# Kernel optimization log

Hardware: AMD Instinct MI355X
Metric: run time of the kernel (lower is better)

The kernel has to match this reference:

```python
import jax, jax.numpy as jnp
import numpy as np
import math

THETA = 10000.0

def apply_rope(x):
    # x: [B, H, S, D] with D even; interleaved even/odd rotation
    B, H, S, D = x.shape
    dim_half = D // 2
    freq_idx = jnp.arange(dim_half, dtype=jnp.float32)
    inv_freq = jnp.exp(-math.log(THETA) * freq_idx * 2.0 / D)  # [D/2]
    pos = jnp.arange(S, dtype=jnp.float32)
    angles = pos[:, None] * inv_freq[None, :]      # [S, D/2]
    cos = jnp.cos(angles)[None, None]              # [1,1,S,D/2]
    sin = jnp.sin(angles)[None, None]
    x_even = x[..., ::2]
    x_odd = x[..., 1::2]
    r_even = x_even * cos - x_odd * sin
    r_odd = x_odd * cos + x_even * sin
    return jnp.stack([r_even, r_odd], axis=-1).reshape(B, H, S, D)

def setup_inputs() -> dict:
    key = jax.random.key(0)
    ks = jax.random.split(key, 5)
    B, S, E = 2, 2048, 1024
    std = 0.02
    inp = {
        "hidden_states": jax.random.normal(ks[0], (B, S, E), dtype=jnp.float32),
        "Wq": jax.random.normal(ks[1], (E, E), dtype=jnp.float32) * std,
        "bq": jnp.zeros((E,), dtype=jnp.float32),
        "Wk": jax.random.normal(ks[2], (E, E), dtype=jnp.float32) * std,
        "bk": jnp.zeros((E,), dtype=jnp.float32),
        "Wv": jax.random.normal(ks[3], (E, E), dtype=jnp.float32) * std,
        "bv": jnp.zeros((E,), dtype=jnp.float32),
        "Wo": jax.random.normal(ks[4], (E, E), dtype=jnp.float32) * std,
        "bo": jnp.zeros((E,), dtype=jnp.float32),
    }
    return inp

def reference(hidden_states, Wq, bq, Wk, bk, Wv, bv, Wo, bo):
    NUM_HEADS = 16
    B, S, E = hidden_states.shape
    D = E // NUM_HEADS
    scale = 1.0 / math.sqrt(D)

    def proj(W, b):
        # torch Linear: x @ W.T + b; then [B,S,H,D] -> [B,H,S,D]
        y = hidden_states @ W.T + b
        return y.reshape(B, S, NUM_HEADS, D).transpose(0, 2, 1, 3)

    q = apply_rope(proj(Wq, bq))
    k = apply_rope(proj(Wk, bk))
    v = proj(Wv, bv)

    scores = jnp.einsum("bhqd,bhkd->bhqk", q, k) * scale
    attn = jax.nn.softmax(scores, axis=-1)
    out = jnp.einsum("bhqk,bhkd->bhqd", attn, v)  # [B,H,S,D]
    out = out.transpose(0, 2, 1, 3).reshape(B, S, E)
    return out @ Wo.T + bo  # dropout: eval mode (identity)
```

## Files before the change

kernel.cpp:

```cpp
#include <hip/hip_runtime.h>
#include <hip/hip_bf16.h>
#include <math.h>

#define B_ 2
#define S_ 2048
#define E_ 1024
#define H_ 16
#define D_ 64
#define M_ (B_*S_)
#define PT 32

typedef short bf16x8 __attribute__((ext_vector_type(8)));
typedef float f32x4 __attribute__((ext_vector_type(4)));
typedef unsigned short u16x4 __attribute__((ext_vector_type(4)));

#define SCLQ 0.18033688011112042f

__device__ __forceinline__ unsigned short f2bf(float f) {
    unsigned int u = __builtin_bit_cast(unsigned int, f);
    u += 0x7FFFu + ((u >> 16) & 1u);
    return (unsigned short)(u >> 16);
}
__device__ __forceinline__ unsigned int pk2bf(float a, float b) {
    __hip_bfloat162 h = __float22bfloat162_rn(make_float2(a, b));
    unsigned int u;
    __builtin_memcpy(&u, &h, 4);
    return u;
}
__device__ __forceinline__ f32x4 mfma16(bf16x8 a, bf16x8 b, f32x4 c) {
    return __builtin_amdgcn_mfma_f32_16x16x32_bf16(a, b, c, 0, 0, 0);
}
__device__ __forceinline__ bf16x8 cvt8(const float* p) {
    f32x4 lo = *(const f32x4*)p;
    f32x4 hi = *(const f32x4*)(p + 4);
    unsigned int pk[4];
    pk[0] = pk2bf(lo[0], lo[1]);
    pk[1] = pk2bf(lo[2], lo[3]);
    pk[2] = pk2bf(hi[0], hi[1]);
    pk[3] = pk2bf(hi[2], hi[3]);
    bf16x8 r;
    __builtin_memcpy(&r, pk, 16);
    return r;
}
__device__ __forceinline__ void g2l16(const unsigned short* g, unsigned short* l) {
    __builtin_amdgcn_global_load_lds(
        (const __attribute__((address_space(1))) unsigned int*)(const void*)g,
        (__attribute__((address_space(3))) unsigned int*)(void*)l,
        16, 0, 0);
}

__global__ __launch_bounds__(256) void cvt_kernel(
    const float* __restrict__ X,  const float* __restrict__ Wq,
    const float* __restrict__ Wk, const float* __restrict__ Wv,
    const float* __restrict__ Wo,
    unsigned short* __restrict__ Xb, unsigned short* __restrict__ Wb,
    float* __restrict__ tab)
{
    const int y = blockIdx.y;
    if (y == 5) {
        unsigned int i = blockIdx.x * 256 + threadIdx.x;
        if (i < 32 * 2048) {
            int f = i >> 11, s = i & 2047;
            const float C = -0.41524101186091903f;
            const float INV2PI = 0.15915494309189535f;
            float inv_rev = exp2f(C * (float)f) * INV2PI;
            float rev = (float)s * inv_rev;
            float fr = rev - rintf(rev);
            tab[i]           = __builtin_amdgcn_cosf(fr);
            tab[65536 + i]   = __builtin_amdgcn_sinf(fr);
        }
        return;
    }
    const float* src = (y == 0) ? X : (y == 1) ? Wq : (y == 2) ? Wk : (y == 3) ? Wv : Wo;
    unsigned short* dst = (y == 0) ? Xb : Wb + (size_t)(y - 1) * (E_ * E_);
    const size_t n = (y == 0) ? (size_t)M_ * E_ : (size_t)E_ * E_;
    size_t i = ((size_t)blockIdx.x * 256 + threadIdx.x) * 8;
    if (i < n) *(bf16x8*)(dst + i) = cvt8(src + i);
}

__global__ __launch_bounds__(256, 4) void qkv_rope_bf(
    const unsigned short* __restrict__ Xb, const unsigned short* __restrict__ Wb,
    const float* __restrict__ bq, const float* __restrict__ bk,
    const float* __restrict__ bv, const float* __restrict__ tab,
    unsigned short* __restrict__ Qo, unsigned short* __restrict__ Ko,
    unsigned short* __restrict__ Vo)
{
    __shared__ __align__(16) unsigned char lds_raw[128 * 132 * 2];
    unsigned short* As = (unsigned short*)lds_raw;
    unsigned short* Bs = (unsigned short*)(lds_raw + 8192);
    unsigned short* Cs = (unsigned short*)lds_raw;

    const int t = threadIdx.x;
    const int w = t >> 6, lane = t & 63, quad = lane >> 4, l16 = lane & 15;
    const int wr = (w >> 1) * 64, wc = (w & 1) * 64;
    const int n0 = blockIdx.x * 128, m0 = blockIdx.y * 128;
    const int z = blockIdx.z;
    const unsigned short* W = Wb + (size_t)z * (E_ * E_);
    const float* bias = (z == 0) ? bq : (z == 1) ? bk : bv;

    const int r4 = t >> 2, c8 = (t & 3) * 8;
    const unsigned short* Ag = Xb + (size_t)(m0 + r4) * E_ + c8;
    const unsigned short* Bg = W  + (size_t)(n0 + r4) * E_ + c8;

    f32x4 zero = {0.f, 0.f, 0.f, 0.f};
    f32x4 acc[4][4];
#pragma unroll
    for (int i = 0; i < 4; i++)
#pragma unroll
        for (int j = 0; j < 4; j++) acc[i][j] = zero;

    for (int kt = 0; kt < E_; kt += 32) {
        __syncthreads();
        g2l16(Ag + kt,           &As[t * 8]);
        g2l16(Ag + 64 * E_ + kt, &As[t * 8 + 2048]);
        g2l16(Bg + kt,           &Bs[t * 8]);
        g2l16(Bg + 64 * E_ + kt, &Bs[t * 8 + 2048]);
        __syncthreads();
        bf16x8 af[4], bfr[4];
#pragma unroll
        for (int i = 0; i < 4; i++)
            af[i] = *(const bf16x8*)&As[(wr + i * 16 + l16) * 32 + quad * 8];
#pragma unroll
        for (int j = 0; j < 4; j++)
            bfr[j] = *(const bf16x8*)&Bs[(wc + j * 16 + l16) * 32 + quad * 8];
#pragma unroll
        for (int i = 0; i < 4; i++)
#pragma unroll
            for (int j = 0; j < 4; j++)
                acc[i][j] = mfma16(af[i], bfr[j], acc[i][j]);
    }

    __syncthreads();
    const int seg = quad;
    if (z < 2) {
        const float qscale = (z == 0) ? SCLQ : 1.0f;
#pragma unroll
        for (int j = 0; j < 4; j++) {
            int n_local = wc + j * 16 + l16;
            int n = n0 + n_local;
            int d = n & 63, f = d >> 1;
            float bvv = bias[n];
            float sgn = (d & 1) ? 1.f : -1.f;
            const float* ct = tab + f * 2048;
            const float* st_ = tab + 65536 + f * 2048;
#pragma unroll
            for (int i = 0; i < 4; i++) {
                int mb = wr + i * 16 + quad * 4;
                int sb = (m0 + mb) & (S_ - 1);
                f32x4 cs4 = *(const f32x4*)&ct[sb];
                f32x4 sn4 = *(const f32x4*)&st_[sb];
#pragma unroll
                for (int r = 0; r < 4; r++) {
                    float val = acc[i][j][r] + bvv;
                    float oth = __shfl_xor(val, 1);
                    Cs[(mb + r) * 132 + n_local] =
                        f2bf((val * cs4[r] + sgn * oth * sn4[r]) * qscale);
                }
            }
        }
        __syncthreads();
        unsigned short* Out = (z == 0) ? Qo : Ko;
        const int btok = m0 >> 11;
        const int half = seg & 1;
#pragma unroll
        for (int it = 0; it < 16; it++) {
            int m_local = it * 8 + w * 2 + (seg >> 1);
            int s = (m0 + m_local) & (S_ - 1);
            int h = (n0 + half * 64) >> 6;
            u16x4 v = *(const u16x4*)&Cs[m_local * 132 + half * 64 + l16 * 4];
            *(u16x4*)&Out[(((size_t)btok * H_ + h) * S_ + s) * D_ + l16 * 4] = v;
        }
    } else {
#pragma unroll
        for (int j = 0; j < 4; j++) {
            int n_local = wc + j * 16 + l16;
            float bvv = bias[n0 + n_local];
#pragma unroll
            for (int i = 0; i < 4; i++) {
                int mb = wr + i * 16 + quad * 4;
#pragma unroll
                for (int r = 0; r < 4; r++)
                    Cs[n_local * 132 + mb + r] = f2bf(acc[i][j][r] + bvv);
            }
        }
        __syncthreads();
        const int btok = m0 >> 11;
        const int s0 = m0 & (S_ - 1);
        const int half = seg & 1;
#pragma unroll
        for (int it = 0; it < 16; it++) {
            int n_local = it * 8 + w * 2 + (seg >> 1);
            int n = n0 + n_local;
            int h = n >> 6, d = n & 63;
            u16x4 v = *(const u16x4*)&Cs[n_local * 132 + half * 64 + l16 * 4];
            *(u16x4*)&Vo[(((size_t)btok * H_ + h) * D_ + d) * S_ + s0 + half * 64 + l16 * 4] = v;
        }
    }
}

__global__ __launch_bounds__(512, 2) void attn_direct(
    const unsigned short* __restrict__ Q, const unsigned short* __restrict__ K,
    const unsigned short* __restrict__ Vt, unsigned short* __restrict__ ctx)
{
    __shared__ unsigned short Ks[3][64 * 64];
    __shared__ unsigned short Vs[3][64 * 64];
    __shared__ unsigned short Ps[8][16 * 72];
    const int t = threadIdx.x;
    const int w = t >> 6, lane = t & 63, quad = lane >> 4, l16 = lane & 15;
    const int bh = blockIdx.y;
    const int q0 = blockIdx.x * 128 + w * 16;
    const int NT = S_ / 64;

    const unsigned short* Qg = Q + ((size_t)bh * S_ + q0) * D_;
    bf16x8 qf[2];
#pragma unroll
    for (int ks = 0; ks < 2; ks++)
        qf[ks] = *(const bf16x8*)(Qg + (size_t)l16 * 64 + ks * 32 + quad * 8);

    bf16x8 ones;
#pragma unroll
    for (int e = 0; e < 8; e++) ones[e] = (short)0x3F80;

    f32x4 zero = {0.f, 0.f, 0.f, 0.f};
    f32x4 acc_o[4];
    f32x4 acc_l = zero;
#pragma unroll
    for (int j = 0; j < 4; j++) acc_o[j] = zero;

    const int tt = t & 255, ksel = t >> 8;
    const int sr = tt >> 2;
    const int sc = ((tt & 3) ^ ((tt >> 3) & 3)) * 8;
    const unsigned short* KgL = K  + (size_t)bh * S_ * D_ + (size_t)sr * 64 + ksel * 32 + sc;
    const unsigned short* VgL = Vt + (size_t)bh * D_ * S_ + (size_t)sr * S_ + ksel * 32 + sc;

    const int sl = (quad ^ ((l16 >> 1) & 3)) * 8;

    g2l16(KgL, &Ks[0][t * 8]);
    g2l16(VgL, &Vs[0][t * 8]);
    __syncthreads();
    g2l16(KgL + 4096, &Ks[1][t * 8]);
    g2l16(VgL + 64,   &Vs[1][t * 8]);
    {
        f32x4 sc4[4];
#pragma unroll
        for (int j = 0; j < 4; j++) sc4[j] = zero;
#pragma unroll
        for (int ks = 0; ks < 2; ks++)
#pragma unroll
            for (int j = 0; j < 4; j++) {
                bf16x8 kf = *(const bf16x8*)&Ks[0][ks * 2048 + (j * 16 + l16) * 32 + sl];
                sc4[j] = mfma16(qf[ks], kf, sc4[j]);
            }
#pragma unroll
        for (int j = 0; j < 4; j++)
#pragma unroll
            for (int r = 0; r < 4; r += 2) {
                float pa = __builtin_amdgcn_exp2f(sc4[j][r]);
                float pb = __builtin_amdgcn_exp2f(sc4[j][r + 1]);
                unsigned int u = pk2bf(pa, pb);
                Ps[w][(quad * 4 + r)     * 72 + j * 16 + l16] = (unsigned short)u;
                Ps[w][(quad * 4 + r + 1) * 72 + j * 16 + l16] = (unsigned short)(u >> 16);
            }
    }

    int bc = 0, bn = 1, bx = 2;
    for (int i = 0; i < NT - 1; ++i) {
        __syncthreads();
        if (i + 2 < NT) {
            g2l16(KgL + (size_t)(i + 2) * 4096, &Ks[bx][t * 8]);
            g2l16(VgL + (i + 2) * 64,           &Vs[bx][t * 8]);
        }
        bf16x8 pf0 = *(const bf16x8*)&Ps[w][l16 * 72 + quad * 8];
        bf16x8 pf1 = *(const bf16x8*)&Ps[w][l16 * 72 + 32 + quad * 8];

        __builtin_amdgcn_s_setprio(1);
        f32x4 scn[4];
#pragma unroll
        for (int j = 0; j < 4; j++) scn[j] = zero;
#pragma unroll
        for (int ks = 0; ks < 2; ks++)
#pragma unroll
            for (int j = 0; j < 4; j++) {
                bf16x8 kf = *(const bf16x8*)&Ks[bn][ks * 2048 + (j * 16 + l16) * 32 + sl];
                scn[j] = mfma16(qf[ks], kf, scn[j]);
            }
#pragma unroll
        for (int jd = 0; jd < 4; jd++) {
            bf16x8 vf = *(const bf16x8*)&Vs[bc][(jd * 16 + l16) * 32 + sl];
            acc_o[jd] = mfma16(pf0, vf, acc_o[jd]);
        }
        acc_l = mfma16(pf0, ones, acc_l);
#pragma unroll
        for (int jd = 0; jd < 4; jd++) {
            bf16x8 vf = *(const bf16x8*)&Vs[bc][2048 + (jd * 16 + l16) * 32 + sl];
            acc_o[jd] = mfma16(pf1, vf, acc_o[jd]);
        }
        acc_l = mfma16(pf1, ones, acc_l);
        __builtin_amdgcn_s_setprio(0);

#pragma unroll
        for (int j = 0; j < 4; j++)
#pragma unroll
            for (int r = 0; r < 4; r += 2) {
                float pa = __builtin_amdgcn_exp2f(scn[j][r]);
                float pb = __builtin_amdgcn_exp2f(scn[j][r + 1]);
                unsigned int u = pk2bf(pa, pb);
                Ps[w][(quad * 4 + r)     * 72 + j * 16 + l16] = (unsigned short)u;
                Ps[w][(quad * 4 + r + 1) * 72 + j * 16 + l16] = (unsigned short)(u >> 16);
            }

        int tb = bc; bc = bn; bn = bx; bx = tb;
    }

    {
        bf16x8 pf0 = *(const bf16x8*)&Ps[w][l16 * 72 + quad * 8];
        bf16x8 pf1 = *(const bf16x8*)&Ps[w][l16 * 72 + 32 + quad * 8];
#pragma unroll
        for (int jd = 0; jd < 4; jd++) {
            bf16x8 vf = *(const bf16x8*)&Vs[bc][(jd * 16 + l16) * 32 + sl];
            acc_o[jd] = mfma16(pf0, vf, acc_o[jd]);
        }
        acc_l = mfma16(pf0, ones, acc_l);
#pragma unroll
        for (int jd = 0; jd < 4; jd++) {
            bf16x8 vf = *(const bf16x8*)&Vs[bc][2048 + (jd * 16 + l16) * 32 + sl];
            acc_o[jd] = mfma16(pf1, vf, acc_o[jd]);
        }
        acc_l = mfma16(pf1, ones, acc_l);
    }

    const int b = bh >> 4, h = bh & 15;
    f32x4 rl;
#pragma unroll
    for (int r = 0; r < 4; r++) rl[r] = 1.0f / acc_l[r];
#pragma unroll
    for (int jd = 0; jd < 4; jd++)
#pragma unroll
        for (int r = 0; r < 4; r++) {
            int qrow = q0 + quad * 4 + r;
            int col = h * 64 + jd * 16 + l16;
            ctx[((size_t)b * S_ + qrow) * E_ + col] = f2bf(acc_o[jd][r] * rl[r]);
        }
}

__global__ __launch_bounds__(256, 4) void out_bf(
    const unsigned short* __restrict__ Cx, const unsigned short* __restrict__ Wob,
    const float* __restrict__ bo, float* __restrict__ out)
{
    __shared__ unsigned short As[128 * 32];
    __shared__ unsigned short Bs[64 * 32];
    const int t = threadIdx.x;
    const int w = t >> 6, lane = t & 63, quad = lane >> 4, l16 = lane & 15;
    const int m0 = blockIdx.y * 128, n0 = blockIdx.x * 64;
    const int wr = w * 32;
    const int r4 = t >> 2, c8 = (t & 3) * 8;
    const unsigned short* Ag = Cx  + (size_t)(m0 + r4) * E_ + c8;
    const unsigned short* Bg = Wob + (size_t)(n0 + r4) * E_ + c8;

    f32x4 zero = {0.f, 0.f, 0.f, 0.f};
    f32x4 acc[2][4];
#pragma unroll
    for (int i = 0; i < 2; i++)
#pragma unroll
        for (int j = 0; j < 4; j++) acc[i][j] = zero;

    for (int kt = 0; kt < E_; kt += 32) {
        __syncthreads();
        g2l16(Ag + kt,           &As[t * 8]);
        g2l16(Ag + 64 * E_ + kt, &As[t * 8 + 2048]);
        g2l16(Bg + kt,           &Bs[t * 8]);
        __syncthreads();
        bf16x8 af[2], bfr[4];
#pragma unroll
        for (int i = 0; i < 2; i++)
            af[i] = *(const bf16x8*)&As[(wr + i * 16 + l16) * 32 + quad * 8];
#pragma unroll
        for (int j = 0; j < 4; j++)
            bfr[j] = *(const bf16x8*)&Bs[(j * 16 + l16) * 32 + quad * 8];
#pragma unroll
        for (int i = 0; i < 2; i++)
#pragma unroll
            for (int j = 0; j < 4; j++)
                acc[i][j] = mfma16(af[i], bfr[j], acc[i][j]);
    }

#pragma unroll
    for (int j = 0; j < 4; j++) {
        int n = n0 + j * 16 + l16;
        float bvv = bo[n];
#pragma unroll
        for (int i = 0; i < 2; i++) {
            int mrow = m0 + wr + i * 16 + quad * 4;
#pragma unroll
            for (int r = 0; r < 4; r++)
                out[(size_t)(mrow + r) * E_ + n] = acc[i][j][r] + bvv;
        }
    }
}

__global__ __launch_bounds__(256, 3) void qkv_rope_f32(
    const float* __restrict__ X,
    const float* __restrict__ Wq, const float* __restrict__ Wk,
    const float* __restrict__ Wv,
    const float* __restrict__ bq, const float* __restrict__ bk,
    const float* __restrict__ bv,
    unsigned short* __restrict__ Qo, unsigned short* __restrict__ Ko,
    unsigned short* __restrict__ Vo)
{
    __shared__ __align__(16) unsigned char lds_raw[128 * 132 * 2];
    unsigned short* As = (unsigned short*)lds_raw;
    unsigned short* Bs = (unsigned short*)(lds_raw + 8192);
    unsigned short* Cs = (unsigned short*)lds_raw;

    const int t = threadIdx.x;
    const int w = t >> 6, lane = t & 63, quad = lane >> 4, l16 = lane & 15;
    const int wr = (w >> 1) * 64, wc = (w & 1) * 64;
    const int n0 = blockIdx.x * 128, m0 = blockIdx.y * 128;
    const int z = blockIdx.z;
    const float* W    = (z == 0) ? Wq : (z == 1) ? Wk : Wv;
    const float* bias = (z == 0) ? bq : (z == 1) ? bk : bv;

    const int r4 = t >> 2, c8 = (t & 3) * 8;
    const int st = r4 * PT + c8;
    const float* Ag = X + (size_t)(m0 + r4) * E_ + c8;
    const float* Bg = W + (size_t)(n0 + r4) * E_ + c8;

    f32x4 zero = {0.f, 0.f, 0.f, 0.f};
    f32x4 acc[4][4];
#pragma unroll
    for (int i = 0; i < 4; i++)
#pragma unroll
        for (int j = 0; j < 4; j++) acc[i][j] = zero;

    for (int kt = 0; kt < E_; kt += 32) {
        bf16x8 a0 = cvt8(Ag + kt);
        bf16x8 a1 = cvt8(Ag + 64 * E_ + kt);
        bf16x8 b0 = cvt8(Bg + kt);
        bf16x8 b1 = cvt8(Bg + 64 * E_ + kt);
        __syncthreads();
        *(bf16x8*)&As[st]           = a0;
        *(bf16x8*)&As[st + 64 * PT] = a1;
        *(bf16x8*)&Bs[st]           = b0;
        *(bf16x8*)&Bs[st + 64 * PT] = b1;
        __syncthreads();
        bf16x8 af[4], bfr[4];
#pragma unroll
        for (int i = 0; i < 4; i++)
            af[i] = *(const bf16x8*)&As[(wr + i * 16 + l16) * PT + quad * 8];
#pragma unroll
        for (int j = 0; j < 4; j++)
            bfr[j] = *(const bf16x8*)&Bs[(wc + j * 16 + l16) * PT + quad * 8];
#pragma unroll
        for (int i = 0; i < 4; i++)
#pragma unroll
            for (int j = 0; j < 4; j++)
                acc[i][j] = mfma16(af[i], bfr[j], acc[i][j]);
    }

    __syncthreads();
    const int seg = quad;
    if (z < 2) {
        const float C = -0.41524101186091903f;
        const float INV2PI = 0.15915494309189535f;
        const float qscale = (z == 0) ? SCLQ : 1.0f;
#pragma unroll
        for (int j = 0; j < 4; j++) {
            int n_local = wc + j * 16 + l16;
            int n = n0 + n_local;
            int d = n & 63, f = d >> 1;
            float inv_rev = exp2f(C * (float)f) * INV2PI;
            float bvv = bias[n];
            float sgn = (d & 1) ? 1.f : -1.f;
#pragma unroll
            for (int i = 0; i < 4; i++) {
                int mb = wr + i * 16 + quad * 4;
#pragma unroll
                for (int r = 0; r < 4; r++) {
                    int m = m0 + mb + r;
                    int s = m & (S_ - 1);
                    float val = acc[i][j][r] + bvv;
                    float oth = __shfl_xor(val, 1);
                    float rev = (float)s * inv_rev;
                    float fr = rev - rintf(rev);
                    float sn = __builtin_amdgcn_sinf(fr);
                    float cs = __builtin_amdgcn_cosf(fr);
                    Cs[(mb + r) * 132 + n_local] =
                        f2bf((val * cs + sgn * oth * sn) * qscale);
                }
            }
        }
        __syncthreads();
        unsigned short* Out = (z == 0) ? Qo : Ko;
        const int btok = m0 >> 11;
        const int half = seg & 1;
#pragma unroll
        for (int it = 0; it < 16; it++) {
            int m_local = it * 8 + w * 2 + (seg >> 1);
            int s = (m0 + m_local) & (S_ - 1);
            int h = (n0 + half * 64) >> 6;
            u16x4 v = *(const u16x4*)&Cs[m_local * 132 + half * 64 + l16 * 4];
            *(u16x4*)&Out[(((size_t)btok * H_ + h) * S_ + s) * D_ + l16 * 4] = v;
        }
    } else {
#pragma unroll
        for (int j = 0; j < 4; j++) {
            int n_local = wc + j * 16 + l16;
            float bvv = bias[n0 + n_local];
#pragma unroll
            for (int i = 0; i < 4; i++) {
                int mb = wr + i * 16 + quad * 4;
#pragma unroll
                for (int r = 0; r < 4; r++)
                    Cs[n_local * 132 + mb + r] = f2bf(acc[i][j][r] + bvv);
            }
        }
        __syncthreads();
        const int btok = m0 >> 11;
        const int s0 = m0 & (S_ - 1);
        const int half = seg & 1;
#pragma unroll
        for (int it = 0; it < 16; it++) {
            int n_local = it * 8 + w * 2 + (seg >> 1);
            int n = n0 + n_local;
            int h = n >> 6, d = n & 63;
            u16x4 v = *(const u16x4*)&Cs[n_local * 132 + half * 64 + l16 * 4];
            *(u16x4*)&Vo[(((size_t)btok * H_ + h) * D_ + d) * S_ + s0 + half * 64 + l16 * 4] = v;
        }
    }
}

__global__ __launch_bounds__(256, 2) void out_f32(
    const unsigned short* __restrict__ Cx, const float* __restrict__ Wo,
    const float* __restrict__ bo, float* __restrict__ out)
{
    __shared__ unsigned short As[128 * PT];
    __shared__ unsigned short Bs[64 * PT];
    const int t = threadIdx.x;
    const int w = t >> 6, lane = t & 63, quad = lane >> 4, l16 = lane & 15;
    const int m0 = blockIdx.y * 128, n0 = blockIdx.x * 64;
    const int wr = w * 32;
    const int r4 = t >> 2, c8 = (t & 3) * 8;
    const int st = r4 * PT + c8;
    const unsigned short* Ag = Cx + (size_t)(m0 + r4) * E_ + c8;
    const float*          Bg = Wo + (size_t)(n0 + (r4 & 63)) * E_ + c8;

    f32x4 zero = {0.f, 0.f, 0.f, 0.f};
    f32x4 acc[2][4];
#pragma unroll
    for (int i = 0; i < 2; i++)
#pragma unroll
        for (int j = 0; j < 4; j++) acc[i][j] = zero;

    for (int kt = 0; kt < E_; kt += 32) {
        bf16x8 a0 = *(const bf16x8*)(Ag + kt);
        bf16x8 a1 = *(const bf16x8*)(Ag + 64 * E_ + kt);
        bf16x8 b0 = cvt8(Bg + kt);
        __syncthreads();
        *(bf16x8*)&As[st]           = a0;
        *(bf16x8*)&As[st + 64 * PT] = a1;
        *(bf16x8*)&Bs[st]           = b0;
        __syncthreads();
        bf16x8 af[2], bfr[4];
#pragma unroll
        for (int i = 0; i < 2; i++)
            af[i] = *(const bf16x8*)&As[(wr + i * 16 + l16) * PT + quad * 8];
#pragma unroll
        for (int j = 0; j < 4; j++)
            bfr[j] = *(const bf16x8*)&Bs[(j * 16 + l16) * PT + quad * 8];
#pragma unroll
        for (int i = 0; i < 2; i++)
#pragma unroll
            for (int j = 0; j < 4; j++)
                acc[i][j] = mfma16(af[i], bfr[j], acc[i][j]);
    }

#pragma unroll
    for (int j = 0; j < 4; j++) {
        int n = n0 + j * 16 + l16;
        float bvv = bo[n];
#pragma unroll
        for (int i = 0; i < 2; i++) {
            int mrow = m0 + wr + i * 16 + quad * 4;
#pragma unroll
            for (int r = 0; r < 4; r++)
                out[(size_t)(mrow + r) * E_ + n] = acc[i][j][r] + bvv;
        }
    }
}

extern "C" void kernel_launch(void* const* d_in, const int* in_sizes, int n_in,
                              void* d_out, int out_size, void* d_ws, size_t ws_size,
                              hipStream_t stream) {
    const float* X  = (const float*)d_in[0];
    const float* Wq = (const float*)d_in[1];
    const float* bq = (const float*)d_in[2];
    const float* Wk = (const float*)d_in[3];
    const float* bk = (const float*)d_in[4];
    const float* Wv = (const float*)d_in[5];
    const float* bv = (const float*)d_in[6];
    const float* Wo = (const float*)d_in[7];
    const float* bo = (const float*)d_in[8];
    float* outp = (float*)d_out;

    const size_t TN = (size_t)B_ * H_ * S_ * D_;
    const size_t need_f32 = 4 * TN * sizeof(unsigned short);
    const size_t need_bf  = 5 * TN * sizeof(unsigned short) + 2 * 65536 * sizeof(float);
    if (ws_size < need_f32) return;

    unsigned short* Qb = (unsigned short*)d_ws;
    unsigned short* Kb = Qb + TN;
    unsigned short* Vb = Kb + TN;

    if (ws_size >= need_bf) {
        unsigned short* Xb = Vb + TN;
        unsigned short* Wb = Xb + TN;
        float* tab = (float*)(Wb + 4 * (size_t)(E_ * E_));
        unsigned short* Cx = Xb;

        cvt_kernel<<<dim3(2048, 6), 256, 0, stream>>>(X, Wq, Wk, Wv, Wo, Xb, Wb, tab);
        qkv_rope_bf<<<dim3(E_ / 128, M_ / 128, 3), 256, 0, stream>>>(
            Xb, Wb, bq, bk, bv, tab, Qb, Kb, Vb);
        attn_direct<<<dim3(S_ / 128, B_ * H_), 512, 0, stream>>>(Qb, Kb, Vb, Cx);
        out_bf<<<dim3(E_ / 64, M_ / 128), 256, 0, stream>>>(
            Cx, Wb + 3 * (size_t)(E_ * E_), bo, outp);
    } else {
        unsigned short* Cx = Vb + TN;
        qkv_rope_f32<<<dim3(E_ / 128, M_ / 128, 3), 256, 0, stream>>>(
            X, Wq, Wk, Wv, bq, bk, bv, Qb, Kb, Vb);
        attn_direct<<<dim3(S_ / 128, B_ * H_), 512, 0, stream>>>(Qb, Kb, Vb, Cx);
        out_f32<<<dim3(E_ / 64, M_ / 128), 256, 0, stream>>>(Cx, Wo, bo, outp);
    }
}
```

Measured before the change: 191.7 us.

## Process two 16-row query groups per wave in attention to reuse K/V fragments

Each wave in the attention kernel now handles 32 query rows (two 16-row groups) instead of 16, and each block covers 256 queries. Every K and V fragment read from LDS feeds two MFMAs, halving LDS fragment traffic per FLOP and halving global K/V tile loads per query. The grid shrinks to 256 blocks, which lowers parallelism on a GPU with many CUs, and register pressure rises from the doubled accumulators.

```diff
diff --git a/kernel.cpp b/kernel.cpp
--- a/kernel.cpp
+++ b/kernel.cpp
@@ -204,28 +204,32 @@
 {
     __shared__ unsigned short Ks[3][64 * 64];
     __shared__ unsigned short Vs[3][64 * 64];
-    __shared__ unsigned short Ps[8][16 * 72];
+    __shared__ unsigned short Ps[8][32 * 72];
     const int t = threadIdx.x;
     const int w = t >> 6, lane = t & 63, quad = lane >> 4, l16 = lane & 15;
     const int bh = blockIdx.y;
-    const int q0 = blockIdx.x * 128 + w * 16;
+    const int q0 = blockIdx.x * 256 + w * 32;
     const int NT = S_ / 64;
 
     const unsigned short* Qg = Q + ((size_t)bh * S_ + q0) * D_;
-    bf16x8 qf[2];
-#pragma unroll
-    for (int ks = 0; ks < 2; ks++)
-        qf[ks] = *(const bf16x8*)(Qg + (size_t)l16 * 64 + ks * 32 + quad * 8);
+    bf16x8 qf[2][2];
+#pragma unroll
+    for (int rg = 0; rg < 2; rg++)
+#pragma unroll
+        for (int ks = 0; ks < 2; ks++)
+            qf[rg][ks] = *(const bf16x8*)(Qg + (size_t)(rg * 16 + l16) * 64 + ks * 32 + quad * 8);
 
     bf16x8 ones;
 #pragma unroll
     for (int e = 0; e < 8; e++) ones[e] = (short)0x3F80;
 
     f32x4 zero = {0.f, 0.f, 0.f, 0.f};
-    f32x4 acc_o[4];
-    f32x4 acc_l = zero;
-#pragma unroll
-    for (int j = 0; j < 4; j++) acc_o[j] = zero;
+    f32x4 acc_o[2][4];
+    f32x4 acc_l[2] = {zero, zero};
+#pragma unroll
+    for (int rg = 0; rg < 2; rg++)
+#pragma unroll
+        for (int j = 0; j < 4; j++) acc_o[rg][j] = zero;
 
     const int tt = t & 255, ksel = t >> 8;
     const int sr = tt >> 2;
@@ -241,26 +245,31 @@
     g2l16(KgL + 4096, &Ks[1][t * 8]);
     g2l16(VgL + 64,   &Vs[1][t * 8]);
     {
-        f32x4 sc4[4];
-#pragma unroll
-        for (int j = 0; j < 4; j++) sc4[j] = zero;
+        f32x4 sc4[2][4];
+#pragma unroll
+        for (int rg = 0; rg < 2; rg++)
+#pragma unroll
+            for (int j = 0; j < 4; j++) sc4[rg][j] = zero;
 #pragma unroll
         for (int ks = 0; ks < 2; ks++)
 #pragma unroll
             for (int j = 0; j < 4; j++) {
                 bf16x8 kf = *(const bf16x8*)&Ks[0][ks * 2048 + (j * 16 + l16) * 32 + sl];
-                sc4[j] = mfma16(qf[ks], kf, sc4[j]);
-            }
-#pragma unroll
-        for (int j = 0; j < 4; j++)
-#pragma unroll
-            for (int r = 0; r < 4; r += 2) {
-                float pa = __builtin_amdgcn_exp2f(sc4[j][r]);
-                float pb = __builtin_amdgcn_exp2f(sc4[j][r + 1]);
-                unsigned int u = pk2bf(pa, pb);
-                Ps[w][(quad * 4 + r)     * 72 + j * 16 + l16] = (unsigned short)u;
-                Ps[w][(quad * 4 + r + 1) * 72 + j * 16 + l16] = (unsigned short)(u >> 16);
-            }
+                sc4[0][j] = mfma16(qf[0][ks], kf, sc4[0][j]);
+                sc4[1][j] = mfma16(qf[1][ks], kf, sc4[1][j]);
+            }
+#pragma unroll
+        for (int rg = 0; rg < 2; rg++)
+#pragma unroll
+            for (int j = 0; j < 4; j++)
+#pragma unroll
+                for (int r = 0; r < 4; r += 2) {
+                    float pa = __builtin_amdgcn_exp2f(sc4[rg][j][r]);
+                    float pb = __builtin_amdgcn_exp2f(sc4[rg][j][r + 1]);
+                    unsigned int u = pk2bf(pa, pb);
+                    Ps[w][(rg * 16 + quad * 4 + r)     * 72 + j * 16 + l16] = (unsigned short)u;
+                    Ps[w][(rg * 16 + quad * 4 + r + 1) * 72 + j * 16 + l16] = (unsigned short)(u >> 16);
+                }
     }
 
     int bc = 0, bn = 1, bx = 2;
@@ -270,77 +279,91 @@
             g2l16(KgL + (size_t)(i + 2) * 4096, &Ks[bx][t * 8]);
             g2l16(VgL + (i + 2) * 64,           &Vs[bx][t * 8]);
         }
-        bf16x8 pf0 = *(const bf16x8*)&Ps[w][l16 * 72 + quad * 8];
-        bf16x8 pf1 = *(const bf16x8*)&Ps[w][l16 * 72 + 32 + quad * 8];
+        bf16x8 pf[2][2];
+#pragma unroll
+        for (int rg = 0; rg < 2; rg++)
+#pragma unroll
+            for (int ks = 0; ks < 2; ks++)
+                pf[rg][ks] = *(const bf16x8*)&Ps[w][(rg * 16 + l16) * 72 + ks * 32 + quad * 8];
 
         __builtin_amdgcn_s_setprio(1);
-        f32x4 scn[4];
-#pragma unroll
-        for (int j = 0; j < 4; j++) scn[j] = zero;
+        f32x4 scn[2][4];
+#pragma unroll
+        for (int rg = 0; rg < 2; rg++)
+#pragma unroll
+            for (int j = 0; j < 4; j++) scn[rg][j] = zero;
 #pragma unroll
         for (int ks = 0; ks < 2; ks++)
 #pragma unroll
             for (int j = 0; j < 4; j++) {
                 bf16x8 kf = *(const bf16x8*)&Ks[bn][ks * 2048 + (j * 16 + l16) * 32 + sl];
-                scn[j] = mfma16(qf[ks], kf, scn[j]);
-            }
-#pragma unroll
-        for (int jd = 0; jd < 4; jd++) {
-            bf16x8 vf = *(const bf16x8*)&Vs[bc][(jd * 16 + l16) * 32 + sl];
-            acc_o[jd] = mfma16(pf0, vf, acc_o[jd]);
-        }
-        acc_l = mfma16(pf0, ones, acc_l);
-#pragma unroll
-        for (int jd = 0; jd < 4; jd++) {
-            bf16x8 vf = *(const bf16x8*)&Vs[bc][2048 + (jd * 16 + l16) * 32 + sl];
-            acc_o[jd] = mfma16(pf1, vf, acc_o[jd]);
-        }
-        acc_l = mfma16(pf1, ones, acc_l);
+                scn[0][j] = mfma16(qf[0][ks], kf, scn[0][j]);
+                scn[1][j] = mfma16(qf[1][ks], kf, scn[1][j]);
+            }
+#pragma unroll
+        for (int ks = 0; ks < 2; ks++) {
+#pragma unroll
+            for (int jd = 0; jd < 4; jd++) {
+                bf16x8 vf = *(const bf16x8*)&Vs[bc][ks * 2048 + (jd * 16 + l16) * 32 + sl];
+                acc_o[0][jd] = mfma16(pf[0][ks], vf, acc_o[0][jd]);
+                acc_o[1][jd] = mfma16(pf[1][ks], vf, acc_o[1][jd]);
+            }
+            acc_l[0] = mfma16(pf[0][ks], ones, acc_l[0]);
+            acc_l[1] = mfma16(pf[1][ks], ones, acc_l[1]);
+        }
         __builtin_amdgcn_s_setprio(0);
 
 #pragma unroll
-        for (int j = 0; j < 4; j++)
-#pragma unroll
-            for (int r = 0; r < 4; r += 2) {
-                float pa = __builtin_amdgcn_exp2f(scn[j][r]);
-                float pb = __builtin_amdgcn_exp2f(scn[j][r + 1]);
-                unsigned int u = pk2bf(pa, pb);
-                Ps[w][(quad * 4 + r)     * 72 + j * 16 + l16] = (unsigned short)u;
-                Ps[w][(quad * 4 + r + 1) * 72 + j * 16 + l16] = (unsigned short)(u >> 16);
-            }
+        for (int rg = 0; rg < 2; rg++)
+#pragma unroll
+            for (int j = 0; j < 4; j++)
+#pragma unroll
+                for (int r = 0; r < 4; r += 2) {
+                    float pa = __builtin_amdgcn_exp2f(scn[rg][j][r]);
+                    float pb = __builtin_amdgcn_exp2f(scn[rg][j][r + 1]);
+                    unsigned int u = pk2bf(pa, pb);
+                    Ps[w][(rg * 16 + quad * 4 + r)     * 72 + j * 16 + l16] = (unsigned short)u;
+                    Ps[w][(rg * 16 + quad * 4 + r + 1) * 72 + j * 16 + l16] = (unsigned short)(u >> 16);
+                }
 
         int tb = bc; bc = bn; bn = bx; bx = tb;
     }
 
     {
-        bf16x8 pf0 = *(const bf16x8*)&Ps[w][l16 * 72 + quad * 8];
-        bf16x8 pf1 = *(const bf16x8*)&Ps[w][l16 * 72 + 32 + quad * 8];
-#pragma unroll
-        for (int jd = 0; jd < 4; jd++) {
-            bf16x8 vf = *(const bf16x8*)&Vs[bc][(jd * 16 + l16) * 32 + sl];
-            acc_o[jd] = mfma16(pf0, vf, acc_o[jd]);
-        }
-        acc_l = mfma16(pf0, ones, acc_l);
-#pragma unroll
-        for (int jd = 0; jd < 4; jd++) {
-            bf16x8 vf = *(const bf16x8*)&Vs[bc][2048 + (jd * 16 + l16) * 32 + sl];
-            acc_o[jd] = mfma16(pf1, vf, acc_o[jd]);
-        }
-        acc_l = mfma16(pf1, ones, acc_l);
+        bf16x8 pf[2][2];
+#pragma unroll
+        for (int rg = 0; rg < 2; rg++)
+#pragma unroll
+            for (int ks = 0; ks < 2; ks++)
+                pf[rg][ks] = *(const bf16x8*)&Ps[w][(rg * 16 + l16) * 72 + ks * 32 + quad * 8];
+#pragma unroll
+        for (int ks = 0; ks < 2; ks++) {
+#pragma unroll
+            for (int jd = 0; jd < 4; jd++) {
+                bf16x8 vf = *(const bf16x8*)&Vs[bc][ks * 2048 + (jd * 16 + l16) * 32 + sl];
+                acc_o[0][jd] = mfma16(pf[0][ks], vf, acc_o[0][jd]);
+                acc_o[1][jd] = mfma16(pf[1][ks], vf, acc_o[1][jd]);
+            }
+            acc_l[0] = mfma16(pf[0][ks], ones, acc_l[0]);
+            acc_l[1] = mfma16(pf[1][ks], ones, acc_l[1]);
+        }
     }
 
     const int b = bh >> 4, h = bh & 15;
-    f32x4 rl;
-#pragma unroll
-    for (int r = 0; r < 4; r++) rl[r] = 1.0f / acc_l[r];
-#pragma unroll
-    for (int jd = 0; jd < 4; jd++)
-#pragma unroll
-        for (int r = 0; r < 4; r++) {
-            int qrow = q0 + quad * 4 + r;
-            int col = h * 64 + jd * 16 + l16;
-            ctx[((size_t)b * S_ + qrow) * E_ + col] = f2bf(acc_o[jd][r] * rl[r]);
-        }
+#pragma unroll
+    for (int rg = 0; rg < 2; rg++) {
+        f32x4 rl;
+#pragma unroll
+        for (int r = 0; r < 4; r++) rl[r] = 1.0f / acc_l[rg][r];
+#pragma unroll
+        for (int jd = 0; jd < 4; jd++)
+#pragma unroll
+            for (int r = 0; r < 4; r++) {
+                int qrow = q0 + rg * 16 + quad * 4 + r;
+                int col = h * 64 + jd * 16 + l16;
+                ctx[((size_t)b * S_ + qrow) * E_ + col] = f2bf(acc_o[rg][jd][r] * rl[r]);
+            }
+    }
 }
 
 __global__ __launch_bounds__(256, 4) void out_bf(
@@ -620,14 +643,14 @@
         cvt_kernel<<<dim3(2048, 6), 256, 0, stream>>>(X, Wq, Wk, Wv, Wo, Xb, Wb, tab);
         qkv_rope_bf<<<dim3(E_ / 128, M_ / 128, 3), 256, 0, stream>>>(
             Xb, Wb, bq, bk, bv, tab, Qb, Kb, Vb);
-        attn_direct<<<dim3(S_ / 128, B_ * H_), 512, 0, stream>>>(Qb, Kb, Vb, Cx);
+        attn_direct<<<dim3(S_ / 256, B_ * H_), 512, 0, stream>>>(Qb, Kb, Vb, Cx);
         out_bf<<<dim3(E_ / 64, M_ / 128), 256, 0, stream>>>(
             Cx, Wb + 3 * (size_t)(E_ * E_), bo, outp);
     } else {
         unsigned short* Cx = Vb + TN;
         qkv_rope_f32<<<dim3(E_ / 128, M_ / 128, 3), 256, 0, stream>>>(
             X, Wq, Wk, Wv, bq, bk, bv, Qb, Kb, Vb);
-        attn_direct<<<dim3(S_ / 128, B_ * H_), 512, 0, stream>>>(Qb, Kb, Vb, Cx);
+        attn_direct<<<dim3(S_ / 256, B_ * H_), 512, 0, stream>>>(Qb, Kb, Vb, Cx);
         out_f32<<<dim3(E_ / 64, M_ / 128), 256, 0, stream>>>(Cx, Wo, bo, outp);
     }
 }
```

After: 197.4 us. 1.03x slower.

## Shrink attention blocks to four waves, double-buffer K/V, swizzle P and block order

Applied to the files above, without the earlier changes.

The attention kernel now runs 256-thread blocks of 64 query rows instead of 512-thread blocks of 128, with twice as many blocks and launch bounds raised to four blocks per CU. K and V move from triple to double buffering, with the V load for the next tile issued one iteration later, which lowers LDS use per block. The P scratch tile now uses an XOR-swizzled 64-wide layout in place of 72-element row padding, and block indices are remapped so that consecutive workgroups spread across heads. The intent is higher occupancy and better L2 locality, at the cost of each K/V tile being loaded by twice as many blocks and less lookahead to hide load latency.

```diff
diff --git a/kernel.cpp b/kernel.cpp
--- a/kernel.cpp
+++ b/kernel.cpp
@@ -198,17 +198,20 @@
     }
 }
 
-__global__ __launch_bounds__(512, 2) void attn_direct(
+__global__ __launch_bounds__(256, 4) void attn_direct(
     const unsigned short* __restrict__ Q, const unsigned short* __restrict__ K,
     const unsigned short* __restrict__ Vt, unsigned short* __restrict__ ctx)
 {
-    __shared__ unsigned short Ks[3][64 * 64];
-    __shared__ unsigned short Vs[3][64 * 64];
-    __shared__ unsigned short Ps[8][16 * 72];
+    __shared__ unsigned short Ks[2][64 * 64];
+    __shared__ unsigned short Vs[2][64 * 64];
+    __shared__ unsigned short Ps[4][16 * 64];
     const int t = threadIdx.x;
     const int w = t >> 6, lane = t & 63, quad = lane >> 4, l16 = lane & 15;
-    const int bh = blockIdx.y;
-    const int q0 = blockIdx.x * 128 + w * 16;
+
+    const int wgid = blockIdx.x + (blockIdx.y << 5);
+    const int sw = (wgid & 7) * 128 + (wgid >> 3);
+    const int bh = sw >> 5;
+    const int q0 = (sw & 31) * 64 + w * 16;
     const int NT = S_ / 64;
 
     const unsigned short* Qg = Q + ((size_t)bh * S_ + q0) * D_;
@@ -227,19 +230,24 @@
 #pragma unroll
     for (int j = 0; j < 4; j++) acc_o[j] = zero;
 
-    const int tt = t & 255, ksel = t >> 8;
-    const int sr = tt >> 2;
-    const int sc = ((tt & 3) ^ ((tt >> 3) & 3)) * 8;
-    const unsigned short* KgL = K  + (size_t)bh * S_ * D_ + (size_t)sr * 64 + ksel * 32 + sc;
-    const unsigned short* VgL = Vt + (size_t)bh * D_ * S_ + (size_t)sr * S_ + ksel * 32 + sc;
+    const int sr = t >> 2;
+    const int sc = ((t & 3) ^ ((t >> 3) & 3)) * 8;
+    const unsigned short* KgL = K  + (size_t)bh * S_ * D_ + (size_t)sr * 64 + sc;
+    const unsigned short* VgL = Vt + (size_t)bh * D_ * S_ + (size_t)sr * S_ + sc;
 
     const int sl = (quad ^ ((l16 >> 1) & 3)) * 8;
-
-    g2l16(KgL, &Ks[0][t * 8]);
-    g2l16(VgL, &Vs[0][t * 8]);
+    const int ps0 = l16 * 64 + ((quad ^ ((l16 >> 1) & 3)) << 3);
+    const int ps1 = l16 * 64 + (((4 + quad) ^ ((l16 >> 1) & 3)) << 3);
+
+#pragma unroll
+    for (int k2 = 0; k2 < 2; k2++) {
+        g2l16(KgL + k2 * 32, &Ks[0][k2 * 2048 + t * 8]);
+        g2l16(VgL + k2 * 32, &Vs[0][k2 * 2048 + t * 8]);
+    }
     __syncthreads();
-    g2l16(KgL + 4096, &Ks[1][t * 8]);
-    g2l16(VgL + 64,   &Vs[1][t * 8]);
+#pragma unroll
+    for (int k2 = 0; k2 < 2; k2++)
+        g2l16(KgL + 4096 + k2 * 32, &Ks[1][k2 * 2048 + t * 8]);
     {
         f32x4 sc4[4];
 #pragma unroll
@@ -252,26 +260,36 @@
                 sc4[j] = mfma16(qf[ks], kf, sc4[j]);
             }
 #pragma unroll
-        for (int j = 0; j < 4; j++)
+        for (int j = 0; j < 4; j++) {
+            int cb = 2 * j + (l16 >> 3);
 #pragma unroll
             for (int r = 0; r < 4; r += 2) {
                 float pa = __builtin_amdgcn_exp2f(sc4[j][r]);
                 float pb = __builtin_amdgcn_exp2f(sc4[j][r + 1]);
                 unsigned int u = pk2bf(pa, pb);
-                Ps[w][(quad * 4 + r)     * 72 + j * 16 + l16] = (unsigned short)u;
-                Ps[w][(quad * 4 + r + 1) * 72 + j * 16 + l16] = (unsigned short)(u >> 16);
-            }
-    }
-
-    int bc = 0, bn = 1, bx = 2;
+                int slot = cb ^ ((quad * 2 + (r >> 1)) & 3);
+                int a0 = (quad * 4 + r) * 64 + slot * 8 + (l16 & 7);
+                Ps[w][a0]      = (unsigned short)u;
+                Ps[w][a0 + 64] = (unsigned short)(u >> 16);
+            }
+        }
+    }
+
     for (int i = 0; i < NT - 1; ++i) {
         __syncthreads();
         if (i + 2 < NT) {
-            g2l16(KgL + (size_t)(i + 2) * 4096, &Ks[bx][t * 8]);
-            g2l16(VgL + (i + 2) * 64,           &Vs[bx][t * 8]);
-        }
-        bf16x8 pf0 = *(const bf16x8*)&Ps[w][l16 * 72 + quad * 8];
-        bf16x8 pf1 = *(const bf16x8*)&Ps[w][l16 * 72 + 32 + quad * 8];
+#pragma unroll
+            for (int k2 = 0; k2 < 2; k2++)
+                g2l16(KgL + (size_t)(i + 2) * 4096 + k2 * 32,
+                      &Ks[i & 1][k2 * 2048 + t * 8]);
+        }
+#pragma unroll
+        for (int k2 = 0; k2 < 2; k2++)
+            g2l16(VgL + (i + 1) * 64 + k2 * 32,
+                  &Vs[(i + 1) & 1][k2 * 2048 + t * 8]);
+
+        bf16x8 pf0 = *(const bf16x8*)&Ps[w][ps0];
+        bf16x8 pf1 = *(const bf16x8*)&Ps[w][ps1];
 
         __builtin_amdgcn_s_setprio(1);
         f32x4 scn[4];
@@ -281,49 +299,52 @@
         for (int ks = 0; ks < 2; ks++)
 #pragma unroll
             for (int j = 0; j < 4; j++) {
-                bf16x8 kf = *(const bf16x8*)&Ks[bn][ks * 2048 + (j * 16 + l16) * 32 + sl];
+                bf16x8 kf = *(const bf16x8*)&Ks[(i + 1) & 1][ks * 2048 + (j * 16 + l16) * 32 + sl];
                 scn[j] = mfma16(qf[ks], kf, scn[j]);
             }
 #pragma unroll
         for (int jd = 0; jd < 4; jd++) {
-            bf16x8 vf = *(const bf16x8*)&Vs[bc][(jd * 16 + l16) * 32 + sl];
+            bf16x8 vf = *(const bf16x8*)&Vs[i & 1][(jd * 16 + l16) * 32 + sl];
             acc_o[jd] = mfma16(pf0, vf, acc_o[jd]);
         }
         acc_l = mfma16(pf0, ones, acc_l);
 #pragma unroll
         for (int jd = 0; jd < 4; jd++) {
-            bf16x8 vf = *(const bf16x8*)&Vs[bc][2048 + (jd * 16 + l16) * 32 + sl];
+            bf16x8 vf = *(const bf16x8*)&Vs[i & 1][2048 + (jd * 16 + l16) * 32 + sl];
             acc_o[jd] = mfma16(pf1, vf, acc_o[jd]);
         }
         acc_l = mfma16(pf1, ones, acc_l);
         __builtin_amdgcn_s_setprio(0);
 
 #pragma unroll
-        for (int j = 0; j < 4; j++)
+        for (int j = 0; j < 4; j++) {
+            int cb = 2 * j + (l16 >> 3);
 #pragma unroll
             for (int r = 0; r < 4; r += 2) {
                 float pa = __builtin_amdgcn_exp2f(scn[j][r]);
                 float pb = __builtin_amdgcn_exp2f(scn[j][r + 1]);
                 unsigned int u = pk2bf(pa, pb);
-                Ps[w][(quad * 4 + r)     * 72 + j * 16 + l16] = (unsigned short)u;
-                Ps[w][(quad * 4 + r + 1) * 72 + j * 16 + l16] = (unsigned short)(u >> 16);
-            }
-
-        int tb = bc; bc = bn; bn = bx; bx = tb;
-    }
-
+                int slot = cb ^ ((quad * 2 + (r >> 1)) & 3);
+                int a0 = (quad * 4 + r) * 64 + slot * 8 + (l16 & 7);
+                Ps[w][a0]      = (unsigned short)u;
+                Ps[w][a0 + 64] = (unsigned short)(u >> 16);
+            }
+        }
+    }
+
+    __syncthreads();
     {
-        bf16x8 pf0 = *(const bf16x8*)&Ps[w][l16 * 72 + quad * 8];
-        bf16x8 pf1 = *(const bf16x8*)&Ps[w][l16 * 72 + 32 + quad * 8];
+        bf16x8 pf0 = *(const bf16x8*)&Ps[w][ps0];
+        bf16x8 pf1 = *(const bf16x8*)&Ps[w][ps1];
 #pragma unroll
         for (int jd = 0; jd < 4; jd++) {
-            bf16x8 vf = *(const bf16x8*)&Vs[bc][(jd * 16 + l16) * 32 + sl];
+            bf16x8 vf = *(const bf16x8*)&Vs[(NT - 1) & 1][(jd * 16 + l16) * 32 + sl];
             acc_o[jd] = mfma16(pf0, vf, acc_o[jd]);
         }
         acc_l = mfma16(pf0, ones, acc_l);
 #pragma unroll
         for (int jd = 0; jd < 4; jd++) {
-            bf16x8 vf = *(const bf16x8*)&Vs[bc][2048 + (jd * 16 + l16) * 32 + sl];
+            bf16x8 vf = *(const bf16x8*)&Vs[(NT - 1) & 1][2048 + (jd * 16 + l16) * 32 + sl];
             acc_o[jd] = mfma16(pf1, vf, acc_o[jd]);
         }
         acc_l = mfma16(pf1, ones, acc_l);
@@ -620,14 +641,14 @@
         cvt_kernel<<<dim3(2048, 6), 256, 0, stream>>>(X, Wq, Wk, Wv, Wo, Xb, Wb, tab);
         qkv_rope_bf<<<dim3(E_ / 128, M_ / 128, 3), 256, 0, stream>>>(
             Xb, Wb, bq, bk, bv, tab, Qb, Kb, Vb);
-        attn_direct<<<dim3(S_ / 128, B_ * H_), 512, 0, stream>>>(Qb, Kb, Vb, Cx);
+        attn_direct<<<dim3(S_ / 64, B_ * H_), 256, 0, stream>>>(Qb, Kb, Vb, Cx);
         out_bf<<<dim3(E_ / 64, M_ / 128), 256, 0, stream>>>(
             Cx, Wb + 3 * (size_t)(E_ * E_), bo, outp);
     } else {
         unsigned short* Cx = Vb + TN;
         qkv_rope_f32<<<dim3(E_ / 128, M_ / 128, 3), 256, 0, stream>>>(
             X, Wq, Wk, Wv, bq, bk, bv, Qb, Kb, Vb);
-        attn_direct<<<dim3(S_ / 128, B_ * H_), 512, 0, stream>>>(Qb, Kb, Vb, Cx);
+        attn_direct<<<dim3(S_ / 64, B_ * H_), 256, 0, stream>>>(Qb, Kb, Vb, Cx);
         out_f32<<<dim3(E_ / 64, M_ / 128), 256, 0, stream>>>(Cx, Wo, bo, outp);
     }
 }
```

New measurement: 199.6 us. 4.1% more time.
